# Performance work log

Measured on AMD Instinct MI355X. Metric: run time of the kernel, lower is better.

Reference implementation:

```python
import jax, jax.numpy as jnp
import numpy as np

B, C, W, H = 4, 128, 64, 64
CK = 32  # f/g projection channels


def setup_inputs() -> dict:
    key = jax.random.key(0)
    ks = jax.random.split(key, 8)
    s_in = 1.0 / np.sqrt(C)
    return {
        "x": jax.random.normal(ks[0], (B, C, W, H), dtype=jnp.float32),
        "Wf": jax.random.normal(ks[1], (CK, C), dtype=jnp.float32) * s_in,
        "bf": jnp.zeros((CK,), dtype=jnp.float32),
        "Wg": jax.random.normal(ks[2], (CK, C), dtype=jnp.float32) * s_in,
        "bg": jnp.zeros((CK,), dtype=jnp.float32),
        "Wh": jax.random.normal(ks[3], (C, C), dtype=jnp.float32) * s_in,
        "bh": jnp.zeros((C,), dtype=jnp.float32),
        "gamma": jax.random.normal(ks[4], (1,), dtype=jnp.float32) * 0.1,
    }


def reference(x, Wf, bf, Wg, bg, Wh, bh, gamma):
    b, c, w, h = x.shape
    n = w * h
    xf = x.reshape(b, c, n)                                  # [B,C,N]
    # 1x1 convs == per-pixel linear projections
    f = jnp.einsum('oc,bcn->bon', Wf, xf) + bf[None, :, None]  # [B,32,N]
    g = jnp.einsum('oc,bcn->bon', Wg, xf) + bg[None, :, None]  # [B,32,N]
    v = jnp.einsum('oc,bcn->bon', Wh, xf) + bh[None, :, None]  # [B,C,N]
    # attention = softmax(f^T g) over last dim (g positions), as in the torch code
    att = jax.nn.softmax(jnp.einsum('bkn,bkm->bnm', f, g), axis=-1)  # [B,N,N]
    # self_attention = h @ attention  (contract over f-position axis)
    sa = jnp.einsum('bcn,bnm->bcm', v, att).reshape(b, c, w, h)
    return gamma[0] * sa + x
```

## Files before the change

### kernel.cpp

```cpp
#include <hip/hip_runtime.h>
#include <hip/hip_bf16.h>

#define BB 4
#define CC 128
#define NN 4096
#define CK 32
#define L2E 1.442695040888963f

typedef __attribute__((ext_vector_type(8))) short short8v;
typedef __attribute__((ext_vector_type(4))) float float4v;

__device__ inline ushort f2bf(float f) {
    union { __hip_bfloat16 h; ushort u; } cv;
    cv.h = __float2bfloat16(f);
    return cv.u;
}
__device__ inline uint pk2(float lo, float hi) {
    return ((uint)f2bf(lo)) | ((uint)f2bf(hi) << 16);
}
__device__ __forceinline__ void gll16(const void* g, void* l) {
    __builtin_amdgcn_global_load_lds(
        (const __attribute__((address_space(1))) void*)g,
        (__attribute__((address_space(3))) void*)l, 16, 0, 0);
}
__device__ __forceinline__ void gll4(const void* g, void* l) {
    __builtin_amdgcn_global_load_lds(
        (const __attribute__((address_space(1))) void*)g,
        (__attribute__((address_space(3))) void*)l, 4, 0, 0);
}

__global__ __launch_bounds__(256) void proj_kernel(
    const float* __restrict__ x,
    const float* __restrict__ Wf, const float* __restrict__ bf,
    const float* __restrict__ Wg, const float* __restrict__ bg,
    const float* __restrict__ Wh, const float* __restrict__ bh,
    const float* __restrict__ gamma,
    ushort* __restrict__ ft, ushort* __restrict__ gt, ushort* __restrict__ vh)
{
    __shared__ float xs[CC][64];
    const int t  = threadIdx.x;
    const int n0 = blockIdx.x * 64;
    const int b  = blockIdx.y;
    const float* xb = x + (size_t)b * CC * NN + n0;

    {
        const int j = t & 63;
        #pragma unroll
        for (int i = 0; i < 32; ++i) {
            const int c = (t >> 6) + 4 * i;
            xs[c][j] = xb[(size_t)c * NN + j];
        }
    }
    __syncthreads();

    const int jq = t & 15;
    const int og = t >> 4;

    float acc[12][4];
    #pragma unroll
    for (int i = 0; i < 12; ++i)
        #pragma unroll
        for (int jj = 0; jj < 4; ++jj) acc[i][jj] = 0.f;

    for (int c = 0; c < CC; ++c) {
        const float4 xv = *reinterpret_cast<const float4*>(&xs[c][jq * 4]);
        #pragma unroll
        for (int i = 0; i < 12; ++i) {
            const int o = og + 16 * i;
            float w;
            if (i < 2)       w = Wf[o * CC + c];
            else if (i < 4)  w = Wg[(o - 32) * CC + c];
            else             w = Wh[(o - 64) * CC + c];
            acc[i][0] += w * xv.x;
            acc[i][1] += w * xv.y;
            acc[i][2] += w * xv.z;
            acc[i][3] += w * xv.w;
        }
    }

    const float sgn = (gamma[0] < 0.f) ? -1.f : 1.f;
    const int n_base = n0 + jq * 4;
    #pragma unroll
    for (int i = 0; i < 2; ++i) {
        const int o = og + 16 * i;
        const float bias = bf[o];
        #pragma unroll
        for (int jj = 0; jj < 4; ++jj)
            ft[((size_t)b * NN + n_base + jj) * CK + o] = f2bf(acc[i][jj] + bias);
    }
    #pragma unroll
    for (int i = 2; i < 4; ++i) {
        const int o = og + 16 * (i - 2);
        const float bias = bg[o];
        #pragma unroll
        for (int jj = 0; jj < 4; ++jj)
            gt[((size_t)b * NN + n_base + jj) * CK + o] = f2bf(acc[i][jj] + bias);
    }
    #pragma unroll
    for (int i = 4; i < 12; ++i) {
        const int c = og + 16 * (i - 4);
        const float bias = bh[c];
        ushort4 pkv;
        pkv.x = f2bf(sgn * (acc[i][0] + bias));
        pkv.y = f2bf(sgn * (acc[i][1] + bias));
        pkv.z = f2bf(sgn * (acc[i][2] + bias));
        pkv.w = f2bf(sgn * (acc[i][3] + bias));
        *reinterpret_cast<ushort4*>(&vh[((size_t)b * CC + c) * NN + n_base]) = pkv;
    }
}

__global__ __launch_bounds__(256) void pass1_kernel(
    const ushort* __restrict__ ft, const ushort* __restrict__ gt,
    float* __restrict__ Dpart)
{
    const int t   = threadIdx.x;
    const int w   = t >> 6;
    const int l   = t & 63;
    const int g16 = l >> 4;
    const int l16 = l & 15;
    const int n0  = blockIdx.x * 64;
    const int b   = blockIdx.y;
    const int mz  = blockIdx.z;

    const ushort* ftb = ft + (size_t)b * NN * CK;
    const ushort* gtb = gt + (size_t)b * NN * CK;

    const short8v afrag = *reinterpret_cast<const short8v*>(
        &ftb[(size_t)(n0 + 16 * w + l16) * CK + 8 * g16]);

    const float4v zf = {0.f, 0.f, 0.f, 0.f};
    float d0 = 0.f, d1 = 0.f, d2 = 0.f, d3 = 0.f;
    const int m0 = mz * 1024;

    short8v bfA = *reinterpret_cast<const short8v*>(
        &gtb[(size_t)(m0 + l16) * CK + 8 * g16]);
    #pragma unroll 1
    for (int mt = 0; mt < 64; mt += 2) {
        const short8v bfB = *reinterpret_cast<const short8v*>(
            &gtb[(size_t)(m0 + (mt + 1) * 16 + l16) * CK + 8 * g16]);
        float4v s = __builtin_amdgcn_mfma_f32_16x16x32_bf16(afrag, bfA, zf, 0, 0, 0);
        d0 += __expf(s[0]); d1 += __expf(s[1]); d2 += __expf(s[2]); d3 += __expf(s[3]);
        bfA = *reinterpret_cast<const short8v*>(
            &gtb[(size_t)(m0 + (((mt + 2) & 63)) * 16 + l16) * CK + 8 * g16]);
        float4v s2 = __builtin_amdgcn_mfma_f32_16x16x32_bf16(afrag, bfB, zf, 0, 0, 0);
        d0 += __expf(s2[0]); d1 += __expf(s2[1]); d2 += __expf(s2[2]); d3 += __expf(s2[3]);
    }
    #pragma unroll
    for (int msk = 1; msk <= 8; msk <<= 1) {
        d0 += __shfl_xor(d0, msk);
        d1 += __shfl_xor(d1, msk);
        d2 += __shfl_xor(d2, msk);
        d3 += __shfl_xor(d3, msk);
    }
    if (l16 < 4) {
        const int n = n0 + 16 * w + 4 * g16 + l16;
        const float v = (l16 == 0) ? d0 : (l16 == 1) ? d1 : (l16 == 2) ? d2 : d3;
        Dpart[((size_t)b * NN + n) * 4 + mz] = v;
    }
}

__global__ __launch_bounds__(256) void reduce_kernel(
    const float* __restrict__ Dpart, float* __restrict__ Ld,
    const float* __restrict__ gamma)
{
    const int i = blockIdx.x * 256 + threadIdx.x;
    const float4 d4 = *reinterpret_cast<const float4*>(&Dpart[(size_t)i * 4]);
    const float D = d4.x + d4.y + d4.z + d4.w;
    Ld[i] = log2f(fabsf(gamma[0])) - log2f(D);
}

#define V_OFF 0
#define F_OFF 4096
#define L_OFF 6144
#define BUFB  6400
#define WSTR  12800

__global__ __launch_bounds__(512) void pass2_kernel(
    const ushort* __restrict__ ft, const ushort* __restrict__ gt,
    const ushort* __restrict__ vh, const float* __restrict__ Ld,
    const float* __restrict__ x, float* __restrict__ out)
{
    __shared__ __align__(16) char smem[8 * WSTR];

    const int t   = threadIdx.x;
    const int w   = t >> 6;
    const int l   = t & 63;
    const int g16 = l >> 4;
    const int l16 = l & 15;
    const int ch  = w & 1;
    const int nq  = w >> 1;

    const int bid = blockIdx.x;
    const int xcd = bid & 7;
    const int b   = xcd >> 1;
    const int m0  = ((bid >> 3) + 32 * (xcd & 1)) * 64;

    const ushort* ftb = ft + (size_t)b * NN * CK;
    const ushort* gtb = gt + (size_t)b * NN * CK;
    const ushort* vhb = vh + (size_t)b * CC * NN;
    const float*  ldb = Ld + (size_t)b * NN;

    char* wsm = smem + w * WSTR;

    short8v gfrag[4];
    #pragma unroll
    for (int tm = 0; tm < 4; ++tm)
        gfrag[tm] = *reinterpret_cast<const short8v*>(
            &gtb[(size_t)(m0 + 16 * tm + l16) * CK + 8 * g16]);

    const float4v zf = {0.f, 0.f, 0.f, 0.f};
    float4v acc[4][4];
    #pragma unroll
    for (int tc = 0; tc < 4; ++tc)
        #pragma unroll
        for (int tm = 0; tm < 4; ++tm) acc[tc][tm] = zf;

    const int nbase = nq * 1024;
    const int rr = l >> 2, cp = l & 3;

#define STAGE(n0_, bo_) do {                                                   \
    _Pragma("unroll")                                                          \
    for (int j = 0; j < 4; ++j) {                                              \
        const int row = j * 16 + rr;                                           \
        gll16(vhb + (size_t)(64 * ch + row) * NN + (n0_)                       \
                  + (((2 * cp) ^ (row & 6)) << 2),                             \
              wsm + (bo_) + V_OFF + j * 1024);                                 \
    }                                                                          \
    _Pragma("unroll")                                                          \
    for (int j = 0; j < 2; ++j) {                                              \
        const int row = j * 16 + rr;                                           \
        gll16(ftb + (size_t)((n0_) + row) * CK + cp * 8,                       \
              wsm + (bo_) + F_OFF + j * 1024);                                 \
    }                                                                          \
    gll4(ldb + (n0_) + (l & 31), wsm + (bo_) + L_OFF);                         \
} while (0)

    STAGE(nbase, 0);
    asm volatile("s_waitcnt vmcnt(0)" ::: "memory");

    int bo = 0;
    #pragma unroll 1
    for (int st = 0; st < 32; ++st) {
        const int n0 = nbase + st * 32;
        if (st < 31) {
            STAGE(n0 + 32, bo ^ BUFB);
            asm volatile("s_waitcnt vmcnt(7)" ::: "memory");
        } else {
            asm volatile("s_waitcnt vmcnt(0)" ::: "memory");
        }

        const char*  Vb = wsm + bo + V_OFF;
        const char*  Fb = wsm + bo + F_OFF;
        const float* Lb = (const float*)(wsm + bo + L_OFF);

        const short8v af0 = *reinterpret_cast<const short8v*>(Fb + l16 * 64 + g16 * 16);
        const short8v af1 = *reinterpret_cast<const short8v*>(Fb + (16 + l16) * 64 + g16 * 16);
        const float4  ld0 = *reinterpret_cast<const float4*>(Lb + 4 * g16);
        const float4  ld1 = *reinterpret_cast<const float4*>(Lb + 16 + 4 * g16);

        union { uint u[4]; short8v s; } pf[4];
        #pragma unroll
        for (int tm = 0; tm < 4; ++tm) {
            float4v s0 = __builtin_amdgcn_mfma_f32_16x16x32_bf16(af0, gfrag[tm], zf, 0, 0, 0);
            float4v s1 = __builtin_amdgcn_mfma_f32_16x16x32_bf16(af1, gfrag[tm], zf, 0, 0, 0);
            pf[tm].u[0] = pk2(__builtin_amdgcn_exp2f(fmaf(s0[0], L2E, ld0.x)),
                              __builtin_amdgcn_exp2f(fmaf(s0[1], L2E, ld0.y)));
            pf[tm].u[1] = pk2(__builtin_amdgcn_exp2f(fmaf(s0[2], L2E, ld0.z)),
                              __builtin_amdgcn_exp2f(fmaf(s0[3], L2E, ld0.w)));
            pf[tm].u[2] = pk2(__builtin_amdgcn_exp2f(fmaf(s1[0], L2E, ld1.x)),
                              __builtin_amdgcn_exp2f(fmaf(s1[1], L2E, ld1.y)));
            pf[tm].u[3] = pk2(__builtin_amdgcn_exp2f(fmaf(s1[2], L2E, ld1.z)),
                              __builtin_amdgcn_exp2f(fmaf(s1[3], L2E, ld1.w)));
        }

        #pragma unroll
        for (int tc = 0; tc < 4; ++tc) {
            const int cl = 16 * tc + l16;
            const uint2 va = *reinterpret_cast<const uint2*>(
                Vb + cl * 64 + 8 * (g16 ^ (cl & 6)));
            const uint2 vb2 = *reinterpret_cast<const uint2*>(
                Vb + cl * 64 + 8 * ((4 + g16) ^ (cl & 6)));
            union { uint u[4]; short8v s; } av;
            av.u[0] = va.x;  av.u[1] = va.y;
            av.u[2] = vb2.x; av.u[3] = vb2.y;
            #pragma unroll
            for (int tm = 0; tm < 4; ++tm)
                acc[tc][tm] = __builtin_amdgcn_mfma_f32_16x16x32_bf16(av.s, pf[tm].s, acc[tc][tm], 0, 0, 0);
        }
        bo ^= BUFB;
    }
#undef STAGE

    __syncthreads();
    float4v* rl = (float4v*)smem;
    if (nq != 0) {
        const int slot = (nq - 1) * 2 + ch;
        #pragma unroll
        for (int tc = 0; tc < 4; ++tc)
            #pragma unroll
            for (int tm = 0; tm < 4; ++tm)
                rl[(slot * 16 + tc * 4 + tm) * 64 + l] = acc[tc][tm];
    }
    __syncthreads();
    if (nq == 0) {
        const float* xb = x   + (size_t)b * CC * NN;
        float*       ob = out + (size_t)b * CC * NN;
        #pragma unroll
        for (int tc = 0; tc < 4; ++tc) {
            #pragma unroll
            for (int tm = 0; tm < 4; ++tm) {
                const int fi = tc * 4 + tm;
                float4v s = acc[tc][tm]
                          + rl[((ch) * 16 + fi) * 64 + l]
                          + rl[((2 + ch) * 16 + fi) * 64 + l]
                          + rl[((4 + ch) * 16 + fi) * 64 + l];
                const int cb = 64 * ch + 16 * tc + 4 * g16;
                const int m  = m0 + 16 * tm + l16;
                #pragma unroll
                for (int r = 0; r < 4; ++r) {
                    const size_t idx = (size_t)(cb + r) * NN + m;
                    ob[idx] = s[r] + xb[idx];
                }
            }
        }
    }
}

extern "C" void kernel_launch(void* const* d_in, const int* in_sizes, int n_in,
                              void* d_out, int out_size, void* d_ws, size_t ws_size,
                              hipStream_t stream)
{
    const float* x     = (const float*)d_in[0];
    const float* Wf    = (const float*)d_in[1];
    const float* bf    = (const float*)d_in[2];
    const float* Wg    = (const float*)d_in[3];
    const float* bg    = (const float*)d_in[4];
    const float* Wh    = (const float*)d_in[5];
    const float* bh    = (const float*)d_in[6];
    const float* gamma = (const float*)d_in[7];

    ushort* ft = (ushort*)d_ws;
    ushort* gt = ft + (size_t)BB * NN * CK;
    ushort* vh = gt + (size_t)BB * NN * CK;
    float* Dpart = (float*)(vh + (size_t)BB * CC * NN);
    float* Ld    = Dpart + (size_t)BB * NN * 4;

    float* out = (float*)d_out;

    proj_kernel<<<dim3(NN / 64, BB), 256, 0, stream>>>(x, Wf, bf, Wg, bg, Wh, bh, gamma, ft, gt, vh);
    pass1_kernel<<<dim3(NN / 64, BB, 4), 256, 0, stream>>>(ft, gt, Dpart);
    reduce_kernel<<<dim3(BB * NN / 256), 256, 0, stream>>>(Dpart, Ld, gamma);
    pass2_kernel<<<dim3(256), 512, 0, stream>>>(ft, gt, vh, Ld, x, out);
}
```

Before: 97.19 us.

## Double waves per pass2 block, split key range finer, tree-reduce partials

pass2 now runs 1024 threads (16 waves) per block, each pair of waves covering 512 key positions instead of 1024. The per-wave partial accumulators are combined with a three-level LDS tree reduction instead of a single-stage sum. The f and log-denominator tiles are now read directly from global memory into registers rather than staged through LDS, which shrinks each stage buffer to the V tile only. pass1 is split into 8 key chunks instead of 4, and the reduce kernel sums 8 partials. The aim is more latency hiding and more parallelism per block, at the cost of extra barriers, direct global loads in the inner loop, and register pressure under the 1024-thread launch bound.

```diff
diff --git a/kernel.cpp b/kernel.cpp
--- a/kernel.cpp
+++ b/kernel.cpp
@@ -22,11 +22,6 @@
     __builtin_amdgcn_global_load_lds(
         (const __attribute__((address_space(1))) void*)g,
         (__attribute__((address_space(3))) void*)l, 16, 0, 0);
-}
-__device__ __forceinline__ void gll4(const void* g, void* l) {
-    __builtin_amdgcn_global_load_lds(
-        (const __attribute__((address_space(1))) void*)g,
-        (__attribute__((address_space(3))) void*)l, 4, 0, 0);
 }
 
 __global__ __launch_bounds__(256) void proj_kernel(
@@ -130,18 +125,18 @@
 
     const float4v zf = {0.f, 0.f, 0.f, 0.f};
     float d0 = 0.f, d1 = 0.f, d2 = 0.f, d3 = 0.f;
-    const int m0 = mz * 1024;
+    const int m0 = mz * 512;
 
     short8v bfA = *reinterpret_cast<const short8v*>(
         &gtb[(size_t)(m0 + l16) * CK + 8 * g16]);
     #pragma unroll 1
-    for (int mt = 0; mt < 64; mt += 2) {
+    for (int mt = 0; mt < 32; mt += 2) {
         const short8v bfB = *reinterpret_cast<const short8v*>(
             &gtb[(size_t)(m0 + (mt + 1) * 16 + l16) * CK + 8 * g16]);
         float4v s = __builtin_amdgcn_mfma_f32_16x16x32_bf16(afrag, bfA, zf, 0, 0, 0);
         d0 += __expf(s[0]); d1 += __expf(s[1]); d2 += __expf(s[2]); d3 += __expf(s[3]);
         bfA = *reinterpret_cast<const short8v*>(
-            &gtb[(size_t)(m0 + (((mt + 2) & 63)) * 16 + l16) * CK + 8 * g16]);
+            &gtb[(size_t)(m0 + (((mt + 2) & 31)) * 16 + l16) * CK + 8 * g16]);
         float4v s2 = __builtin_amdgcn_mfma_f32_16x16x32_bf16(afrag, bfB, zf, 0, 0, 0);
         d0 += __expf(s2[0]); d1 += __expf(s2[1]); d2 += __expf(s2[2]); d3 += __expf(s2[3]);
     }
@@ -155,7 +150,7 @@
     if (l16 < 4) {
         const int n = n0 + 16 * w + 4 * g16 + l16;
         const float v = (l16 == 0) ? d0 : (l16 == 1) ? d1 : (l16 == 2) ? d2 : d3;
-        Dpart[((size_t)b * NN + n) * 4 + mz] = v;
+        Dpart[((size_t)b * NN + n) * 8 + mz] = v;
     }
 }
 
@@ -164,23 +159,21 @@
     const float* __restrict__ gamma)
 {
     const int i = blockIdx.x * 256 + threadIdx.x;
-    const float4 d4 = *reinterpret_cast<const float4*>(&Dpart[(size_t)i * 4]);
-    const float D = d4.x + d4.y + d4.z + d4.w;
+    const float4 a4 = *reinterpret_cast<const float4*>(&Dpart[(size_t)i * 8]);
+    const float4 b4 = *reinterpret_cast<const float4*>(&Dpart[(size_t)i * 8 + 4]);
+    const float D = (a4.x + a4.y + a4.z + a4.w) + (b4.x + b4.y + b4.z + b4.w);
     Ld[i] = log2f(fabsf(gamma[0])) - log2f(D);
 }
 
-#define V_OFF 0
-#define F_OFF 4096
-#define L_OFF 6144
-#define BUFB  6400
-#define WSTR  12800
-
-__global__ __launch_bounds__(512) void pass2_kernel(
+#define BUFB  4096
+#define WSTR  8192
+
+__global__ __launch_bounds__(1024, 4) void pass2_kernel(
     const ushort* __restrict__ ft, const ushort* __restrict__ gt,
     const ushort* __restrict__ vh, const float* __restrict__ Ld,
     const float* __restrict__ x, float* __restrict__ out)
 {
-    __shared__ __align__(16) char smem[8 * WSTR];
+    __shared__ __align__(16) char smem[16 * WSTR];
 
     const int t   = threadIdx.x;
     const int w   = t >> 6;
@@ -215,7 +208,7 @@
         #pragma unroll
         for (int tm = 0; tm < 4; ++tm) acc[tc][tm] = zf;
 
-    const int nbase = nq * 1024;
+    const int nbase = nq * 512;
     const int rr = l >> 2, cp = l & 3;
 
 #define STAGE(n0_, bo_) do {                                                   \
@@ -224,15 +217,8 @@
         const int row = j * 16 + rr;                                           \
         gll16(vhb + (size_t)(64 * ch + row) * NN + (n0_)                       \
                   + (((2 * cp) ^ (row & 6)) << 2),                             \
-              wsm + (bo_) + V_OFF + j * 1024);                                 \
+              wsm + (bo_) + j * 1024);                                         \
     }                                                                          \
-    _Pragma("unroll")                                                          \
-    for (int j = 0; j < 2; ++j) {                                              \
-        const int row = j * 16 + rr;                                           \
-        gll16(ftb + (size_t)((n0_) + row) * CK + cp * 8,                       \
-              wsm + (bo_) + F_OFF + j * 1024);                                 \
-    }                                                                          \
-    gll4(ldb + (n0_) + (l & 31), wsm + (bo_) + L_OFF);                         \
 } while (0)
 
     STAGE(nbase, 0);
@@ -240,23 +226,24 @@
 
     int bo = 0;
     #pragma unroll 1
-    for (int st = 0; st < 32; ++st) {
+    for (int st = 0; st < 16; ++st) {
         const int n0 = nbase + st * 32;
-        if (st < 31) {
+
+        const short8v af0 = *reinterpret_cast<const short8v*>(
+            &ftb[(size_t)(n0 + l16) * CK + 8 * g16]);
+        const short8v af1 = *reinterpret_cast<const short8v*>(
+            &ftb[(size_t)(n0 + 16 + l16) * CK + 8 * g16]);
+        const float4 ld0 = *reinterpret_cast<const float4*>(&ldb[n0 + 4 * g16]);
+        const float4 ld1 = *reinterpret_cast<const float4*>(&ldb[n0 + 16 + 4 * g16]);
+
+        if (st < 15) {
             STAGE(n0 + 32, bo ^ BUFB);
-            asm volatile("s_waitcnt vmcnt(7)" ::: "memory");
+            asm volatile("s_waitcnt vmcnt(4)" ::: "memory");
         } else {
             asm volatile("s_waitcnt vmcnt(0)" ::: "memory");
         }
 
-        const char*  Vb = wsm + bo + V_OFF;
-        const char*  Fb = wsm + bo + F_OFF;
-        const float* Lb = (const float*)(wsm + bo + L_OFF);
-
-        const short8v af0 = *reinterpret_cast<const short8v*>(Fb + l16 * 64 + g16 * 16);
-        const short8v af1 = *reinterpret_cast<const short8v*>(Fb + (16 + l16) * 64 + g16 * 16);
-        const float4  ld0 = *reinterpret_cast<const float4*>(Lb + 4 * g16);
-        const float4  ld1 = *reinterpret_cast<const float4*>(Lb + 16 + 4 * g16);
+        const char* Vb = wsm + bo;
 
         union { uint u[4]; short8v s; } pf[4];
         #pragma unroll
@@ -276,7 +263,7 @@
         #pragma unroll
         for (int tc = 0; tc < 4; ++tc) {
             const int cl = 16 * tc + l16;
-            const uint2 va = *reinterpret_cast<const uint2*>(
+            const uint2 va  = *reinterpret_cast<const uint2*>(
                 Vb + cl * 64 + 8 * (g16 ^ (cl & 6)));
             const uint2 vb2 = *reinterpret_cast<const uint2*>(
                 Vb + cl * 64 + 8 * ((4 + g16) ^ (cl & 6)));
@@ -291,15 +278,50 @@
     }
 #undef STAGE
 
-    __syncthreads();
     float4v* rl = (float4v*)smem;
-    if (nq != 0) {
-        const int slot = (nq - 1) * 2 + ch;
+    __syncthreads();
+    if (nq >= 4) {
+        const int slot = (nq - 4) * 2 + ch;
         #pragma unroll
         for (int tc = 0; tc < 4; ++tc)
             #pragma unroll
             for (int tm = 0; tm < 4; ++tm)
                 rl[(slot * 16 + tc * 4 + tm) * 64 + l] = acc[tc][tm];
+    }
+    __syncthreads();
+    if (nq < 4) {
+        const int slot = nq * 2 + ch;
+        #pragma unroll
+        for (int tc = 0; tc < 4; ++tc)
+            #pragma unroll
+            for (int tm = 0; tm < 4; ++tm)
+                acc[tc][tm] += rl[(slot * 16 + tc * 4 + tm) * 64 + l];
+    }
+    __syncthreads();
+    if (nq == 2 || nq == 3) {
+        const int slot = (nq - 2) * 2 + ch;
+        #pragma unroll
+        for (int tc = 0; tc < 4; ++tc)
+            #pragma unroll
+            for (int tm = 0; tm < 4; ++tm)
+                rl[(slot * 16 + tc * 4 + tm) * 64 + l] = acc[tc][tm];
+    }
+    __syncthreads();
+    if (nq < 2) {
+        const int slot = nq * 2 + ch;
+        #pragma unroll
+        for (int tc = 0; tc < 4; ++tc)
+            #pragma unroll
+            for (int tm = 0; tm < 4; ++tm)
+                acc[tc][tm] += rl[(slot * 16 + tc * 4 + tm) * 64 + l];
+    }
+    __syncthreads();
+    if (nq == 1) {
+        #pragma unroll
+        for (int tc = 0; tc < 4; ++tc)
+            #pragma unroll
+            for (int tm = 0; tm < 4; ++tm)
+                rl[(ch * 16 + tc * 4 + tm) * 64 + l] = acc[tc][tm];
     }
     __syncthreads();
     if (nq == 0) {
@@ -309,11 +331,7 @@
         for (int tc = 0; tc < 4; ++tc) {
             #pragma unroll
             for (int tm = 0; tm < 4; ++tm) {
-                const int fi = tc * 4 + tm;
-                float4v s = acc[tc][tm]
-                          + rl[((ch) * 16 + fi) * 64 + l]
-                          + rl[((2 + ch) * 16 + fi) * 64 + l]
-                          + rl[((4 + ch) * 16 + fi) * 64 + l];
+                float4v s = acc[tc][tm] + rl[(ch * 16 + tc * 4 + tm) * 64 + l];
                 const int cb = 64 * ch + 16 * tc + 4 * g16;
                 const int m  = m0 + 16 * tm + l16;
                 #pragma unroll
@@ -343,12 +361,12 @@
     ushort* gt = ft + (size_t)BB * NN * CK;
     ushort* vh = gt + (size_t)BB * NN * CK;
     float* Dpart = (float*)(vh + (size_t)BB * CC * NN);
-    float* Ld    = Dpart + (size_t)BB * NN * 4;
+    float* Ld    = Dpart + (size_t)BB * NN * 8;
 
     float* out = (float*)d_out;
 
     proj_kernel<<<dim3(NN / 64, BB), 256, 0, stream>>>(x, Wf, bf, Wg, bg, Wh, bh, gamma, ft, gt, vh);
-    pass1_kernel<<<dim3(NN / 64, BB, 4), 256, 0, stream>>>(ft, gt, Dpart);
+    pass1_kernel<<<dim3(NN / 64, BB, 8), 256, 0, stream>>>(ft, gt, Dpart);
     reduce_kernel<<<dim3(BB * NN / 256), 256, 0, stream>>>(Dpart, Ld, gamma);
-    pass2_kernel<<<dim3(256), 512, 0, stream>>>(ft, gt, vh, Ld, x, out);
-}
+    pass2_kernel<<<dim3(256), 1024, 0, stream>>>(ft, gt, vh, Ld, x, out);
+}
```

Result: slower. 99.18 us (+2.0%).

## Widen projection blocks to 1024 threads and split softmax denominator pass eightfold

Applied to the files above, without the earlier changes.

The projection kernel now runs 1024 threads per block. Each thread computes 3 output rows instead of 12, and the weights are loaded as float4 vectors along the channel axis. The denominator pass splits the key axis into 8 chunks instead of 4, which doubles the grid so more work is in flight, and the reduce kernel sums the 8 partials. The aim is to cut per-thread serial work and raise occupancy in the two front kernels. In exchange, each block holds more registers and the partials buffer doubles in size.

```diff
diff --git a/kernel.cpp b/kernel.cpp
--- a/kernel.cpp
+++ b/kernel.cpp
@@ -29,7 +29,7 @@
         (__attribute__((address_space(3))) void*)l, 4, 0, 0);
 }
 
-__global__ __launch_bounds__(256) void proj_kernel(
+__global__ __launch_bounds__(1024) void proj_kernel(
     const float* __restrict__ x,
     const float* __restrict__ Wf, const float* __restrict__ bf,
     const float* __restrict__ Wg, const float* __restrict__ bg,
@@ -44,68 +44,76 @@
     const float* xb = x + (size_t)b * CC * NN + n0;
 
     {
-        const int j = t & 63;
-        #pragma unroll
-        for (int i = 0; i < 32; ++i) {
-            const int c = (t >> 6) + 4 * i;
-            xs[c][j] = xb[(size_t)c * NN + j];
-        }
+        const int j  = t & 63;
+        const int cb = t >> 6;
+        #pragma unroll
+        for (int i = 0; i < 8; ++i)
+            xs[cb + 16 * i][j] = xb[(size_t)(cb + 16 * i) * NN + j];
     }
     __syncthreads();
 
     const int jq = t & 15;
-    const int og = t >> 4;
-
-    float acc[12][4];
-    #pragma unroll
-    for (int i = 0; i < 12; ++i)
-        #pragma unroll
-        for (int jj = 0; jj < 4; ++jj) acc[i][jj] = 0.f;
-
-    for (int c = 0; c < CC; ++c) {
-        const float4 xv = *reinterpret_cast<const float4*>(&xs[c][jq * 4]);
-        #pragma unroll
-        for (int i = 0; i < 12; ++i) {
-            const int o = og + 16 * i;
-            float w;
-            if (i < 2)       w = Wf[o * CC + c];
-            else if (i < 4)  w = Wg[(o - 32) * CC + c];
-            else             w = Wh[(o - 64) * CC + c];
-            acc[i][0] += w * xv.x;
-            acc[i][1] += w * xv.y;
-            acc[i][2] += w * xv.z;
-            acc[i][3] += w * xv.w;
+    const int og = (t >> 4) & 15;
+    const int i3 = t >> 8;
+
+    const float* wrow[3];
+    float biasv[3];
+    int   mode[3], oc[3];
+    #pragma unroll
+    for (int ii = 0; ii < 3; ++ii) {
+        const int i = i3 * 3 + ii;
+        if (i < 2)      { oc[ii] = og + 16 * i;       wrow[ii] = Wf + oc[ii] * CC; biasv[ii] = bf[oc[ii]]; mode[ii] = 0; }
+        else if (i < 4) { oc[ii] = og + 16 * (i - 2); wrow[ii] = Wg + oc[ii] * CC; biasv[ii] = bg[oc[ii]]; mode[ii] = 1; }
+        else            { oc[ii] = og + 16 * (i - 4); wrow[ii] = Wh + oc[ii] * CC; biasv[ii] = bh[oc[ii]]; mode[ii] = 2; }
+    }
+
+    float acc[3][4];
+    #pragma unroll
+    for (int ii = 0; ii < 3; ++ii)
+        #pragma unroll
+        for (int jj = 0; jj < 4; ++jj) acc[ii][jj] = 0.f;
+
+    #pragma unroll 4
+    for (int c4 = 0; c4 < 32; ++c4) {
+        float4 wv[3];
+        #pragma unroll
+        for (int ii = 0; ii < 3; ++ii)
+            wv[ii] = *reinterpret_cast<const float4*>(&wrow[ii][c4 * 4]);
+        #pragma unroll
+        for (int q = 0; q < 4; ++q) {
+            const float4 xv = *reinterpret_cast<const float4*>(&xs[c4 * 4 + q][jq * 4]);
+            #pragma unroll
+            for (int ii = 0; ii < 3; ++ii) {
+                const float wq = (q == 0) ? wv[ii].x : (q == 1) ? wv[ii].y
+                               : (q == 2) ? wv[ii].z : wv[ii].w;
+                acc[ii][0] += wq * xv.x;
+                acc[ii][1] += wq * xv.y;
+                acc[ii][2] += wq * xv.z;
+                acc[ii][3] += wq * xv.w;
+            }
         }
     }
 
     const float sgn = (gamma[0] < 0.f) ? -1.f : 1.f;
     const int n_base = n0 + jq * 4;
     #pragma unroll
-    for (int i = 0; i < 2; ++i) {
-        const int o = og + 16 * i;
-        const float bias = bf[o];
-        #pragma unroll
-        for (int jj = 0; jj < 4; ++jj)
-            ft[((size_t)b * NN + n_base + jj) * CK + o] = f2bf(acc[i][jj] + bias);
-    }
-    #pragma unroll
-    for (int i = 2; i < 4; ++i) {
-        const int o = og + 16 * (i - 2);
-        const float bias = bg[o];
-        #pragma unroll
-        for (int jj = 0; jj < 4; ++jj)
-            gt[((size_t)b * NN + n_base + jj) * CK + o] = f2bf(acc[i][jj] + bias);
-    }
-    #pragma unroll
-    for (int i = 4; i < 12; ++i) {
-        const int c = og + 16 * (i - 4);
-        const float bias = bh[c];
-        ushort4 pkv;
-        pkv.x = f2bf(sgn * (acc[i][0] + bias));
-        pkv.y = f2bf(sgn * (acc[i][1] + bias));
-        pkv.z = f2bf(sgn * (acc[i][2] + bias));
-        pkv.w = f2bf(sgn * (acc[i][3] + bias));
-        *reinterpret_cast<ushort4*>(&vh[((size_t)b * CC + c) * NN + n_base]) = pkv;
+    for (int ii = 0; ii < 3; ++ii) {
+        if (mode[ii] == 0) {
+            #pragma unroll
+            for (int jj = 0; jj < 4; ++jj)
+                ft[((size_t)b * NN + n_base + jj) * CK + oc[ii]] = f2bf(acc[ii][jj] + biasv[ii]);
+        } else if (mode[ii] == 1) {
+            #pragma unroll
+            for (int jj = 0; jj < 4; ++jj)
+                gt[((size_t)b * NN + n_base + jj) * CK + oc[ii]] = f2bf(acc[ii][jj] + biasv[ii]);
+        } else {
+            ushort4 pkv;
+            pkv.x = f2bf(sgn * (acc[ii][0] + biasv[ii]));
+            pkv.y = f2bf(sgn * (acc[ii][1] + biasv[ii]));
+            pkv.z = f2bf(sgn * (acc[ii][2] + biasv[ii]));
+            pkv.w = f2bf(sgn * (acc[ii][3] + biasv[ii]));
+            *reinterpret_cast<ushort4*>(&vh[((size_t)b * CC + oc[ii]) * NN + n_base]) = pkv;
+        }
     }
 }
 
@@ -130,18 +138,18 @@
 
     const float4v zf = {0.f, 0.f, 0.f, 0.f};
     float d0 = 0.f, d1 = 0.f, d2 = 0.f, d3 = 0.f;
-    const int m0 = mz * 1024;
+    const int m0 = mz * 512;
 
     short8v bfA = *reinterpret_cast<const short8v*>(
         &gtb[(size_t)(m0 + l16) * CK + 8 * g16]);
     #pragma unroll 1
-    for (int mt = 0; mt < 64; mt += 2) {
+    for (int mt = 0; mt < 32; mt += 2) {
         const short8v bfB = *reinterpret_cast<const short8v*>(
             &gtb[(size_t)(m0 + (mt + 1) * 16 + l16) * CK + 8 * g16]);
         float4v s = __builtin_amdgcn_mfma_f32_16x16x32_bf16(afrag, bfA, zf, 0, 0, 0);
         d0 += __expf(s[0]); d1 += __expf(s[1]); d2 += __expf(s[2]); d3 += __expf(s[3]);
         bfA = *reinterpret_cast<const short8v*>(
-            &gtb[(size_t)(m0 + (((mt + 2) & 63)) * 16 + l16) * CK + 8 * g16]);
+            &gtb[(size_t)(m0 + (((mt + 2) & 31)) * 16 + l16) * CK + 8 * g16]);
         float4v s2 = __builtin_amdgcn_mfma_f32_16x16x32_bf16(afrag, bfB, zf, 0, 0, 0);
         d0 += __expf(s2[0]); d1 += __expf(s2[1]); d2 += __expf(s2[2]); d3 += __expf(s2[3]);
     }
@@ -155,7 +163,7 @@
     if (l16 < 4) {
         const int n = n0 + 16 * w + 4 * g16 + l16;
         const float v = (l16 == 0) ? d0 : (l16 == 1) ? d1 : (l16 == 2) ? d2 : d3;
-        Dpart[((size_t)b * NN + n) * 4 + mz] = v;
+        Dpart[((size_t)b * NN + n) * 8 + mz] = v;
     }
 }
 
@@ -164,8 +172,9 @@
     const float* __restrict__ gamma)
 {
     const int i = blockIdx.x * 256 + threadIdx.x;
-    const float4 d4 = *reinterpret_cast<const float4*>(&Dpart[(size_t)i * 4]);
-    const float D = d4.x + d4.y + d4.z + d4.w;
+    const float4 a4 = *reinterpret_cast<const float4*>(&Dpart[(size_t)i * 8]);
+    const float4 b4 = *reinterpret_cast<const float4*>(&Dpart[(size_t)i * 8 + 4]);
+    const float D = (a4.x + a4.y + a4.z + a4.w) + (b4.x + b4.y + b4.z + b4.w);
     Ld[i] = log2f(fabsf(gamma[0])) - log2f(D);
 }
 
@@ -343,12 +352,12 @@
     ushort* gt = ft + (size_t)BB * NN * CK;
     ushort* vh = gt + (size_t)BB * NN * CK;
     float* Dpart = (float*)(vh + (size_t)BB * CC * NN);
-    float* Ld    = Dpart + (size_t)BB * NN * 4;
+    float* Ld    = Dpart + (size_t)BB * NN * 8;
 
     float* out = (float*)d_out;
 
-    proj_kernel<<<dim3(NN / 64, BB), 256, 0, stream>>>(x, Wf, bf, Wg, bg, Wh, bh, gamma, ft, gt, vh);
-    pass1_kernel<<<dim3(NN / 64, BB, 4), 256, 0, stream>>>(ft, gt, Dpart);
+    proj_kernel<<<dim3(NN / 64, BB), 1024, 0, stream>>>(x, Wf, bf, Wg, bg, Wh, bh, gamma, ft, gt, vh);
+    pass1_kernel<<<dim3(NN / 64, BB, 8), 256, 0, stream>>>(ft, gt, Dpart);
     reduce_kernel<<<dim3(BB * NN / 256), 256, 0, stream>>>(Dpart, Ld, gamma);
     pass2_kernel<<<dim3(256), 512, 0, stream>>>(ft, gt, vh, Ld, x, out);
 }
```

New measurement: 87.15 us. -10.3%, faster.
